# Performance work log

Measured on AMD Instinct MI355X. Metric: run time of the kernel, lower is better.

## Reference

```python
import jax, jax.numpy as jnp
import numpy as np

B, T, HKV, HD = 16, 4096, 8, 128
DM, HQ = 4096, 32
CHUNK, TOPK, WINDOW = 64, 16, 512
EPS = 1e-6


def _rms(x, w):
    v = jnp.mean(x * x, axis=-1, keepdims=True)
    return w * (x * jax.lax.rsqrt(v + EPS))


def setup_inputs() -> dict:
    key = jax.random.key(0)
    ks = jax.random.split(key, 12)
    s = 0.02
    return {
        'hidden_states': jax.random.normal(ks[0], (B, 1, DM), jnp.float32),
        'k_cache': jax.random.normal(ks[1], (B, T, HKV, HD), jnp.float32),
        'v_cache': jax.random.normal(ks[2], (B, T, HKV, HD), jnp.float32),
        'lse_swa': jax.random.normal(ks[3], (B, HQ), jnp.float32) * 2.0,
        'Wq': jax.random.normal(ks[4], (DM, DM), jnp.float32) * s,
        'bq': jnp.zeros((DM,), jnp.float32),
        'Wo': jax.random.normal(ks[5], (DM, DM), jnp.float32) * s,
        'bo': jnp.zeros((DM,), jnp.float32),
        'qn_w': jnp.ones((HD,), jnp.float32),
        'lmkn_w': jnp.ones((HD,), jnp.float32),
        'seq_lens': jax.random.randint(ks[6], (B,), T // 2, T + 1).astype(jnp.int32),
    }


def reference(hidden_states, k_cache, v_cache, lse_swa, Wq, bq, Wo, bo, qn_w, lmkn_w, seq_lens):
    g = HQ // HKV  # GQA group size
    scale = 1.0 / np.sqrt(HD).astype(np.float32)
    sl = seq_lens.astype(jnp.int32)

    # q projection + per-head RMSNorm   [B, HQ, HD]
    q = (hidden_states[:, 0] @ Wq + bq).reshape(B, HQ, HD)
    q = _rms(q, qn_w)

    # landmarks: stride-chunk sample of key cache + RMSNorm  [B, C, HKV, HD]
    lmks = _rms(k_cache[:, ::CHUNK], lmkn_w)
    C = lmks.shape[1]

    # landmark scores with GQA grouping  [B, HQ, C]
    ql = q.reshape(B, HKV, g, HD)
    s = (jnp.einsum('bkgd,bckd->bkgc', ql, lmks) * scale).reshape(B, HQ, C)

    # chunk validity: fully inside sequence and outside sliding window
    cs = jnp.arange(C) * CHUNK
    valid = (cs[None, :] + CHUNK <= sl[:, None]) & (cs[None, :] < sl[:, None] - WINDOW)
    s = jnp.where(valid[:, None, :], s, -1e9)

    # top-k chunk routing per query head
    scores, indices = jax.lax.top_k(s, TOPK)  # [B, HQ, TOPK]

    # chunk weights: softmax over [topk scores, swa lse]
    cw = jax.nn.softmax(jnp.concatenate([scores, lse_swa[..., None]], axis=-1), axis=-1)

    # gather selected KV blocks  [B, HQ, TOPK*CHUNK, HD]
    pos = (indices[..., None] * CHUNK + jnp.arange(CHUNK)).reshape(B, HQ, TOPK * CHUNK)
    b_idx = jnp.arange(B)[:, None, None]
    kv_idx = (jnp.arange(HQ) // g)[None, :, None]
    kg = k_cache[b_idx, pos, kv_idx]
    vg = v_cache[b_idx, pos, kv_idx]

    # per-chunk softmax attention
    att = (jnp.einsum('bhd,bhtd->bht', q, kg) * scale).reshape(B, HQ, TOPK, CHUNK)
    tok_valid = (pos < sl[:, None, None]).reshape(B, HQ, TOPK, CHUNK)
    att = jnp.where(tok_valid, att, -1e9)
    p = jax.nn.softmax(att, axis=-1)
    oc = jnp.einsum('bhkc,bhkcd->bhkd', p, vg.reshape(B, HQ, TOPK, CHUNK, HD))

    # weighted combine of chunk outputs + SWA branch (source uses q as swa output)
    hsa_o = jnp.einsum('bhk,bhkd->bhd', cw[:, :, :TOPK], oc)
    swa_o = q * cw[:, :, -1][..., None]
    o = (hsa_o + swa_o).reshape(B, 1, DM)
    return o @ Wo + bo
```

## Files before the change

### kernel.cpp

```cpp
#include <hip/hip_runtime.h>
#include <hip/hip_bf16.h>

#define B_ 16
#define T_ 4096
#define HKV_ 8
#define HD_ 128
#define DM_ 4096
#define HQ_ 32
#define G_ 4
#define CHUNK_ 64
#define TOPK_ 16
#define WINDOW_ 512
#define NC_ 64
#define EPS_ 1e-6f

#define SPLITK 32
#define KCH (DM_ / SPLITK)

__global__ __launch_bounds__(256) void gemm16_splitk(
    const float* __restrict__ A, const float* __restrict__ W,
    const float* __restrict__ bias, float* __restrict__ C)
{
  int n = blockIdx.x * 256 + threadIdx.x;
  int k0 = blockIdx.y * KCH;
  float acc[B_];
  if (blockIdx.y == 0) {
    float bv = bias[n];
#pragma unroll
    for (int b = 0; b < B_; b++) acc[b] = bv;
  } else {
#pragma unroll
    for (int b = 0; b < B_; b++) acc[b] = 0.f;
  }
  const float* Wp = W + (size_t)k0 * DM_ + n;
  for (int kk = 0; kk < KCH; kk++) {
    float w = Wp[(size_t)kk * DM_];
#pragma unroll
    for (int b = 0; b < B_; b++) acc[b] += A[b * DM_ + k0 + kk] * w;
  }
#pragma unroll
  for (int b = 0; b < B_; b++) atomicAdd(&C[b * DM_ + n], acc[b]);
}

__global__ __launch_bounds__(256) void lmk_topk_kernel(
    const float* __restrict__ q_raw, const float* __restrict__ k_cache,
    const float* __restrict__ lse_swa, const float* __restrict__ qn_w,
    const float* __restrict__ lmkn_w, const int* __restrict__ seq_lens,
    float* __restrict__ q_norm, float* __restrict__ cw_ws, int* __restrict__ idx_ws)
{
  int blk = blockIdx.x;
  int b = blk / HKV_, kv = blk % HKV_;
  int tid = threadIdx.x;
  int w = tid >> 6, lane = tid & 63;
  int qh = kv * G_ + w;

  __shared__ float qs[G_][HD_];
  __shared__ float sS[G_][NC_];

  {
    int d0 = lane * 2;
    const float* qp = q_raw + ((size_t)b * HQ_ + qh) * HD_;
    float v0 = qp[d0], v1 = qp[d0 + 1];
    float ss = v0 * v0 + v1 * v1;
#pragma unroll
    for (int off = 1; off < 64; off <<= 1) ss += __shfl_xor(ss, off);
    float rs = rsqrtf(ss * (1.0f / HD_) + EPS_);
    float n0 = v0 * rs * qn_w[d0], n1 = v1 * rs * qn_w[d0 + 1];
    qs[w][d0] = n0; qs[w][d0 + 1] = n1;
    float* qo = q_norm + ((size_t)b * HQ_ + qh) * HD_;
    qo[d0] = n0; qo[d0 + 1] = n1;
  }
  __syncthreads();

  const float scale = 0.088388347648318447f;

  for (int c = w; c < NC_; c += 4) {
    int d0 = lane * 2;
    const float* kp = k_cache + (((size_t)b * T_ + c * CHUNK_) * HKV_ + kv) * HD_;
    float v0 = kp[d0], v1 = kp[d0 + 1];
    float ss = v0 * v0 + v1 * v1;
#pragma unroll
    for (int off = 1; off < 64; off <<= 1) ss += __shfl_xor(ss, off);
    float rs = rsqrtf(ss * (1.0f / HD_) + EPS_);
    float l0 = v0 * rs * lmkn_w[d0], l1 = v1 * rs * lmkn_w[d0 + 1];
#pragma unroll
    for (int gi = 0; gi < G_; gi++) {
      float p = l0 * qs[gi][d0] + l1 * qs[gi][d0 + 1];
#pragma unroll
      for (int off = 1; off < 64; off <<= 1) p += __shfl_xor(p, off);
      if (lane == 0) sS[gi][c] = p * scale;
    }
  }
  __syncthreads();

  {
    int sl = seq_lens[b];
    int cs = lane * CHUNK_;
    float s = sS[w][lane];
    bool valid = (cs + CHUNK_ <= sl) && (cs < sl - WINDOW_);
    if (!valid) s = -1e9f;

    float topv[TOPK_]; int topi[TOPK_];
    float cur = s;
    for (int j = 0; j < TOPK_; j++) {
      float v = cur; int ix = lane;
#pragma unroll
      for (int off = 1; off < 64; off <<= 1) {
        float ov = __shfl_xor(v, off);
        int oi = __shfl_xor(ix, off);
        if (ov > v || (ov == v && oi < ix)) { v = ov; ix = oi; }
      }
      topv[j] = v; topi[j] = ix;
      if (lane == ix) cur = -INFINITY;
    }

    float lse = lse_swa[b * HQ_ + qh];
    float m = lse;
#pragma unroll
    for (int j = 0; j < TOPK_; j++) m = fmaxf(m, topv[j]);
    float sum = expf(lse - m);
    float e[TOPK_];
#pragma unroll
    for (int j = 0; j < TOPK_; j++) { e[j] = expf(topv[j] - m); sum += e[j]; }
    float inv = 1.0f / sum;
    if (lane == 0) {
      float* cwp = cw_ws + ((size_t)b * HQ_ + qh) * (TOPK_ + 1);
      int* ip = idx_ws + ((size_t)b * HQ_ + qh) * TOPK_;
#pragma unroll
      for (int j = 0; j < TOPK_; j++) { cwp[j] = e[j] * inv; ip[j] = topi[j]; }
      cwp[TOPK_] = expf(lse - m) * inv;
    }
  }
}

__global__ __launch_bounds__(256) void attn_kernel(
    const float* __restrict__ q_norm, const float* __restrict__ k_cache,
    const float* __restrict__ v_cache, const float* __restrict__ cw_ws,
    const int* __restrict__ idx_ws, float* __restrict__ o_mid)
{
  int bh = blockIdx.x;
  int b = bh >> 5, h = bh & 31;
  int kvh = h >> 2;
  int tid = threadIdx.x;

  __shared__ float qs[HD_];
  __shared__ float pS[CHUNK_];
  __shared__ float accS[HD_];

  if (tid < HD_) qs[tid] = q_norm[(size_t)bh * HD_ + tid];
  __syncthreads();

  const float scale = 0.088388347648318447f;
  const float* cwp = cw_ws + (size_t)bh * (TOPK_ + 1);
  const int* ip = idx_ws + (size_t)bh * TOPK_;

  int t = tid >> 2, q4 = tid & 3;
  int d = tid & 127, tp = tid >> 7;
  float acc = 0.f;

  for (int k = 0; k < TOPK_; k++) {
    int c = ip[k];
    float cwk = cwp[k];
    int tok0 = c * CHUNK_;
    {
      const float4* krow = (const float4*)(k_cache + (((size_t)b * T_ + tok0 + t) * HKV_ + kvh) * HD_);
      const float4* qp4 = (const float4*)qs;
      float part = 0.f;
#pragma unroll
      for (int i = 0; i < 8; i++) {
        float4 k4 = krow[q4 * 8 + i];
        float4 qv = qp4[q4 * 8 + i];
        part += k4.x * qv.x + k4.y * qv.y + k4.z * qv.z + k4.w * qv.w;
      }
      part += __shfl_xor(part, 1);
      part += __shfl_xor(part, 2);
      if (q4 == 0) pS[t] = part * scale;
    }
    __syncthreads();
    if (tid < 64) {
      float s = pS[tid];
      float m = s;
#pragma unroll
      for (int off = 1; off < 64; off <<= 1) m = fmaxf(m, __shfl_xor(m, off));
      float e2 = expf(s - m);
      float sum = e2;
#pragma unroll
      for (int off = 1; off < 64; off <<= 1) sum += __shfl_xor(sum, off);
      pS[tid] = e2 / sum;
    }
    __syncthreads();
    {
      const float* vbase = v_cache + (((size_t)b * T_ + tok0) * HKV_ + kvh) * HD_ + d;
      float tmp = 0.f;
      int tstart = tp * 32;
#pragma unroll 8
      for (int tt = tstart; tt < tstart + 32; tt++) {
        tmp += pS[tt] * vbase[(size_t)tt * (HKV_ * HD_)];
      }
      acc += cwk * tmp;
    }
    __syncthreads();
  }
  if (tp == 1) accS[d] = acc;
  __syncthreads();
  if (tp == 0) {
    float cw16 = cwp[TOPK_];
    float o = acc + accS[d] + qs[d] * cw16;
    o_mid[(size_t)bh * HD_ + d] = o;
  }
}

extern "C" void kernel_launch(void* const* d_in, const int* in_sizes, int n_in,
                              void* d_out, int out_size, void* d_ws, size_t ws_size,
                              hipStream_t stream)
{
  const float* hidden  = (const float*)d_in[0];
  const float* k_cache = (const float*)d_in[1];
  const float* v_cache = (const float*)d_in[2];
  const float* lse_swa = (const float*)d_in[3];
  const float* Wq      = (const float*)d_in[4];
  const float* bq      = (const float*)d_in[5];
  const float* Wo      = (const float*)d_in[6];
  const float* bo      = (const float*)d_in[7];
  const float* qn_w    = (const float*)d_in[8];
  const float* lmkn_w  = (const float*)d_in[9];
  const int*   seq_lens = (const int*)d_in[10];
  float* out = (float*)d_out;

  float* q_raw  = (float*)d_ws;
  float* q_norm = q_raw + B_ * HQ_ * HD_;
  float* o_mid  = q_norm + B_ * HQ_ * HD_;
  float* cw_ws  = o_mid + B_ * HQ_ * HD_;
  int*   idx_ws = (int*)(cw_ws + B_ * HQ_ * (TOPK_ + 1));

  hipMemsetAsync(q_raw, 0, B_ * DM_ * sizeof(float), stream);
  hipMemsetAsync(d_out, 0, B_ * DM_ * sizeof(float), stream);

  dim3 gg(DM_ / 256, SPLITK);
  gemm16_splitk<<<gg, 256, 0, stream>>>(hidden, Wq, bq, q_raw);
  lmk_topk_kernel<<<B_ * HKV_, 256, 0, stream>>>(q_raw, k_cache, lse_swa, qn_w,
                                                 lmkn_w, seq_lens, q_norm, cw_ws, idx_ws);
  attn_kernel<<<B_ * HQ_, 256, 0, stream>>>(q_norm, k_cache, v_cache, cw_ws, idx_ws, o_mid);
  gemm16_splitk<<<gg, 256, 0, stream>>>(o_mid, Wo, bo, out);
}
```

Measured before the change: 762.6 us.

## Split attention per chunk, widen landmark kernel, replace atomic split-K with reduction

Result: faster. 693.2 us (-9.1%).

```diff
diff --git a/kernel.cpp b/kernel.cpp
--- a/kernel.cpp
+++ b/kernel.cpp
@@ -17,32 +17,39 @@
 #define SPLITK 32
 #define KCH (DM_ / SPLITK)
 
-__global__ __launch_bounds__(256) void gemm16_splitk(
-    const float* __restrict__ A, const float* __restrict__ W,
-    const float* __restrict__ bias, float* __restrict__ C)
+__global__ __launch_bounds__(256) void gemm16_partial(
+    const float* __restrict__ A, const float* __restrict__ W, float* __restrict__ P)
 {
   int n = blockIdx.x * 256 + threadIdx.x;
   int k0 = blockIdx.y * KCH;
   float acc[B_];
-  if (blockIdx.y == 0) {
-    float bv = bias[n];
-#pragma unroll
-    for (int b = 0; b < B_; b++) acc[b] = bv;
-  } else {
-#pragma unroll
-    for (int b = 0; b < B_; b++) acc[b] = 0.f;
-  }
+#pragma unroll
+  for (int b = 0; b < B_; b++) acc[b] = 0.f;
   const float* Wp = W + (size_t)k0 * DM_ + n;
+  const float* Ap = A + k0;
+#pragma unroll 8
   for (int kk = 0; kk < KCH; kk++) {
     float w = Wp[(size_t)kk * DM_];
 #pragma unroll
-    for (int b = 0; b < B_; b++) acc[b] += A[b * DM_ + k0 + kk] * w;
-  }
-#pragma unroll
-  for (int b = 0; b < B_; b++) atomicAdd(&C[b * DM_ + n], acc[b]);
-}
-
-__global__ __launch_bounds__(256) void lmk_topk_kernel(
+    for (int b = 0; b < B_; b++) acc[b] += Ap[b * DM_ + kk] * w;
+  }
+  float* Pp = P + ((size_t)blockIdx.y * B_) * DM_ + n;
+#pragma unroll
+  for (int b = 0; b < B_; b++) Pp[(size_t)b * DM_] = acc[b];
+}
+
+__global__ __launch_bounds__(256) void gemm16_reduce(
+    const float* __restrict__ P, const float* __restrict__ bias, float* __restrict__ C)
+{
+  int i = blockIdx.x * 256 + threadIdx.x;
+  int b = i >> 12, n = i & (DM_ - 1);
+  float s = bias[n];
+#pragma unroll
+  for (int ky = 0; ky < SPLITK; ky++) s += P[(size_t)(ky * B_ + b) * DM_ + n];
+  C[i] = s;
+}
+
+__global__ __launch_bounds__(1024) void lmk_topk_kernel(
     const float* __restrict__ q_raw, const float* __restrict__ k_cache,
     const float* __restrict__ lse_swa, const float* __restrict__ qn_w,
     const float* __restrict__ lmkn_w, const int* __restrict__ seq_lens,
@@ -52,13 +59,29 @@
   int b = blk / HKV_, kv = blk % HKV_;
   int tid = threadIdx.x;
   int w = tid >> 6, lane = tid & 63;
-  int qh = kv * G_ + w;
+  int d0 = lane * 2;
 
   __shared__ float qs[G_][HD_];
   __shared__ float sS[G_][NC_];
 
-  {
-    int d0 = lane * 2;
+  const float scale = 0.088388347648318447f;
+  float lw0 = lmkn_w[d0], lw1 = lmkn_w[d0 + 1];
+
+  float l0[4], l1[4];
+#pragma unroll
+  for (int j = 0; j < 4; j++) {
+    int c = w + 16 * j;
+    const float2* kp = (const float2*)(k_cache + (((size_t)b * T_ + c * CHUNK_) * HKV_ + kv) * HD_);
+    float2 v = kp[lane];
+    float ss = v.x * v.x + v.y * v.y;
+#pragma unroll
+    for (int off = 1; off < 64; off <<= 1) ss += __shfl_xor(ss, off);
+    float rs = rsqrtf(ss * (1.0f / HD_) + EPS_);
+    l0[j] = v.x * rs * lw0;
+    l1[j] = v.y * rs * lw1;
+  }
+  if (w < G_) {
+    int qh = kv * G_ + w;
     const float* qp = q_raw + ((size_t)b * HQ_ + qh) * HD_;
     float v0 = qp[d0], v1 = qp[d0 + 1];
     float ss = v0 * v0 + v1 * v1;
@@ -72,20 +95,12 @@
   }
   __syncthreads();
 
-  const float scale = 0.088388347648318447f;
-
-  for (int c = w; c < NC_; c += 4) {
-    int d0 = lane * 2;
-    const float* kp = k_cache + (((size_t)b * T_ + c * CHUNK_) * HKV_ + kv) * HD_;
-    float v0 = kp[d0], v1 = kp[d0 + 1];
-    float ss = v0 * v0 + v1 * v1;
-#pragma unroll
-    for (int off = 1; off < 64; off <<= 1) ss += __shfl_xor(ss, off);
-    float rs = rsqrtf(ss * (1.0f / HD_) + EPS_);
-    float l0 = v0 * rs * lmkn_w[d0], l1 = v1 * rs * lmkn_w[d0 + 1];
+#pragma unroll
+  for (int j = 0; j < 4; j++) {
+    int c = w + 16 * j;
 #pragma unroll
     for (int gi = 0; gi < G_; gi++) {
-      float p = l0 * qs[gi][d0] + l1 * qs[gi][d0 + 1];
+      float p = l0[j] * qs[gi][d0] + l1[j] * qs[gi][d0 + 1];
 #pragma unroll
       for (int off = 1; off < 64; off <<= 1) p += __shfl_xor(p, off);
       if (lane == 0) sS[gi][c] = p * scale;
@@ -93,7 +108,8 @@
   }
   __syncthreads();
 
-  {
+  if (w < G_) {
+    int qh = kv * G_ + w;
     int sl = seq_lens[b];
     int cs = lane * CHUNK_;
     float s = sS[w][lane];
@@ -133,81 +149,98 @@
   }
 }
 
-__global__ __launch_bounds__(256) void attn_kernel(
+__global__ __launch_bounds__(256) void attn_chunk(
     const float* __restrict__ q_norm, const float* __restrict__ k_cache,
     const float* __restrict__ v_cache, const float* __restrict__ cw_ws,
-    const int* __restrict__ idx_ws, float* __restrict__ o_mid)
-{
-  int bh = blockIdx.x;
+    const int* __restrict__ idx_ws, float* __restrict__ part_o)
+{
+  int blk = blockIdx.x;
+  int bh = blk >> 4, k = blk & (TOPK_ - 1);
   int b = bh >> 5, h = bh & 31;
   int kvh = h >> 2;
   int tid = threadIdx.x;
 
   __shared__ float qs[HD_];
   __shared__ float pS[CHUNK_];
+  __shared__ float Vs[CHUNK_][HD_];
   __shared__ float accS[HD_];
 
+  int c = idx_ws[bh * TOPK_ + k];
+  float cwk = cw_ws[bh * (TOPK_ + 1) + k];
+  int tok0 = c * CHUNK_;
+  const float* Kbase = k_cache + (((size_t)b * T_ + tok0) * HKV_ + kvh) * HD_;
+  const float* Vbase = v_cache + (((size_t)b * T_ + tok0) * HKV_ + kvh) * HD_;
+  const int rowstride = HKV_ * HD_;
+
   if (tid < HD_) qs[tid] = q_norm[(size_t)bh * HD_ + tid];
-  __syncthreads();
-
-  const float scale = 0.088388347648318447f;
-  const float* cwp = cw_ws + (size_t)bh * (TOPK_ + 1);
-  const int* ip = idx_ws + (size_t)bh * TOPK_;
-
-  int t = tid >> 2, q4 = tid & 3;
-  int d = tid & 127, tp = tid >> 7;
-  float acc = 0.f;
-
-  for (int k = 0; k < TOPK_; k++) {
-    int c = ip[k];
-    float cwk = cwp[k];
-    int tok0 = c * CHUNK_;
-    {
-      const float4* krow = (const float4*)(k_cache + (((size_t)b * T_ + tok0 + t) * HKV_ + kvh) * HD_);
-      const float4* qp4 = (const float4*)qs;
-      float part = 0.f;
-#pragma unroll
-      for (int i = 0; i < 8; i++) {
-        float4 k4 = krow[q4 * 8 + i];
-        float4 qv = qp4[q4 * 8 + i];
-        part += k4.x * qv.x + k4.y * qv.y + k4.z * qv.z + k4.w * qv.w;
-      }
-      part += __shfl_xor(part, 1);
-      part += __shfl_xor(part, 2);
-      if (q4 == 0) pS[t] = part * scale;
-    }
+
+  float4 vreg[8];
+#pragma unroll
+  for (int i = 0; i < 8; i++) {
+    int f = i * 256 + tid;
+    int tok = f >> 5, d4 = f & 31;
+    vreg[i] = *(const float4*)(Vbase + (size_t)tok * rowstride + d4 * 4);
+  }
+  __syncthreads();
+
+  {
+    int t = tid >> 2, q4 = tid & 3;
+    const float4* krow = (const float4*)(Kbase + (size_t)t * rowstride);
+    const float4* qp4 = (const float4*)qs;
+    float part = 0.f;
+#pragma unroll
+    for (int i = 0; i < 8; i++) {
+      float4 k4 = krow[q4 * 8 + i];
+      float4 qv = qp4[q4 * 8 + i];
+      part += k4.x * qv.x + k4.y * qv.y + k4.z * qv.z + k4.w * qv.w;
+    }
+    part += __shfl_xor(part, 1);
+    part += __shfl_xor(part, 2);
+    if (q4 == 0) pS[t] = part * 0.088388347648318447f;
+  }
+#pragma unroll
+  for (int i = 0; i < 8; i++) {
+    int f = i * 256 + tid;
+    int tok = f >> 5, d4 = f & 31;
+    *(float4*)&Vs[tok][d4 * 4] = vreg[i];
+  }
+  __syncthreads();
+
+  if (tid < 64) {
+    float s = pS[tid];
+    float m = s;
+#pragma unroll
+    for (int off = 1; off < 64; off <<= 1) m = fmaxf(m, __shfl_xor(m, off));
+    float e2 = expf(s - m);
+    float sum = e2;
+#pragma unroll
+    for (int off = 1; off < 64; off <<= 1) sum += __shfl_xor(sum, off);
+    pS[tid] = e2 / sum;
+  }
+  __syncthreads();
+
+  {
+    int d = tid & 127, tp = tid >> 7;
+    float acc = 0.f;
+#pragma unroll
+    for (int tt = 0; tt < 32; tt++) acc += pS[tp * 32 + tt] * Vs[tp * 32 + tt][d];
+    if (tp) accS[d] = acc;
     __syncthreads();
-    if (tid < 64) {
-      float s = pS[tid];
-      float m = s;
-#pragma unroll
-      for (int off = 1; off < 64; off <<= 1) m = fmaxf(m, __shfl_xor(m, off));
-      float e2 = expf(s - m);
-      float sum = e2;
-#pragma unroll
-      for (int off = 1; off < 64; off <<= 1) sum += __shfl_xor(sum, off);
-      pS[tid] = e2 / sum;
-    }
-    __syncthreads();
-    {
-      const float* vbase = v_cache + (((size_t)b * T_ + tok0) * HKV_ + kvh) * HD_ + d;
-      float tmp = 0.f;
-      int tstart = tp * 32;
-#pragma unroll 8
-      for (int tt = tstart; tt < tstart + 32; tt++) {
-        tmp += pS[tt] * vbase[(size_t)tt * (HKV_ * HD_)];
-      }
-      acc += cwk * tmp;
-    }
-    __syncthreads();
-  }
-  if (tp == 1) accS[d] = acc;
-  __syncthreads();
-  if (tp == 0) {
-    float cw16 = cwp[TOPK_];
-    float o = acc + accS[d] + qs[d] * cw16;
-    o_mid[(size_t)bh * HD_ + d] = o;
-  }
+    if (!tp) part_o[((size_t)bh * TOPK_ + k) * HD_ + d] = cwk * (acc + accS[d]);
+  }
+}
+
+__global__ __launch_bounds__(128) void combine_kernel(
+    const float* __restrict__ part_o, const float* __restrict__ q_norm,
+    const float* __restrict__ cw_ws, float* __restrict__ o_mid)
+{
+  int bh = blockIdx.x;
+  int d = threadIdx.x;
+  float s = 0.f;
+#pragma unroll
+  for (int k = 0; k < TOPK_; k++) s += part_o[((size_t)bh * TOPK_ + k) * HD_ + d];
+  s += q_norm[(size_t)bh * HD_ + d] * cw_ws[bh * (TOPK_ + 1) + TOPK_];
+  o_mid[(size_t)bh * HD_ + d] = s;
 }
 
 extern "C" void kernel_launch(void* const* d_in, const int* in_sizes, int n_in,
@@ -227,19 +260,21 @@
   const int*   seq_lens = (const int*)d_in[10];
   float* out = (float*)d_out;
 
-  float* q_raw  = (float*)d_ws;
-  float* q_norm = q_raw + B_ * HQ_ * HD_;
-  float* o_mid  = q_norm + B_ * HQ_ * HD_;
-  float* cw_ws  = o_mid + B_ * HQ_ * HD_;
+  float* part1  = (float*)d_ws;
+  float* part_o = part1 + (size_t)SPLITK * B_ * DM_;
+  float* q_raw  = part_o + (size_t)B_ * HQ_ * TOPK_ * HD_;
+  float* q_norm = q_raw + B_ * DM_;
+  float* o_mid  = q_norm + B_ * DM_;
+  float* cw_ws  = o_mid + B_ * DM_;
   int*   idx_ws = (int*)(cw_ws + B_ * HQ_ * (TOPK_ + 1));
 
-  hipMemsetAsync(q_raw, 0, B_ * DM_ * sizeof(float), stream);
-  hipMemsetAsync(d_out, 0, B_ * DM_ * sizeof(float), stream);
-
   dim3 gg(DM_ / 256, SPLITK);
-  gemm16_splitk<<<gg, 256, 0, stream>>>(hidden, Wq, bq, q_raw);
-  lmk_topk_kernel<<<B_ * HKV_, 256, 0, stream>>>(q_raw, k_cache, lse_swa, qn_w,
-                                                 lmkn_w, seq_lens, q_norm, cw_ws, idx_ws);
-  attn_kernel<<<B_ * HQ_, 256, 0, stream>>>(q_norm, k_cache, v_cache, cw_ws, idx_ws, o_mid);
-  gemm16_splitk<<<gg, 256, 0, stream>>>(o_mid, Wo, bo, out);
-}
+  gemm16_partial<<<gg, 256, 0, stream>>>(hidden, Wq, part1);
+  gemm16_reduce<<<B_ * DM_ / 256, 256, 0, stream>>>(part1, bq, q_raw);
+  lmk_topk_kernel<<<B_ * HKV_, 1024, 0, stream>>>(q_raw, k_cache, lse_swa, qn_w,
+                                                  lmkn_w, seq_lens, q_norm, cw_ws, idx_ws);
+  attn_chunk<<<B_ * HQ_ * TOPK_, 256, 0, stream>>>(q_norm, k_cache, v_cache, cw_ws, idx_ws, part_o);
+  combine_kernel<<<B_ * HQ_, 128, 0, stream>>>(part_o, q_norm, cw_ws, o_mid);
+  gemm16_partial<<<gg, 256, 0, stream>>>(o_mid, Wo, part1);
+  gemm16_reduce<<<B_ * DM_ / 256, 256, 0, stream>>>(part1, bo, out);
+}
```
